# Kernel optimization log

Hardware: AMD Instinct MI355X
Metric: run time of the kernel (lower is better)

## Reference

```python
import jax, jax.numpy as jnp
import numpy as np
import math

B, T, C = 2, 2048, 1024
H, DK, DV = 16, 64, 64


def setup_inputs() -> dict:
    key = jax.random.key(0)
    ks = jax.random.split(key, 5)
    # randw(*d) = randn(*d) / sqrt(d[-1])
    x = jax.random.normal(ks[0], (B, T, C), dtype=jnp.float32)
    w_q = jax.random.normal(ks[1], (H, DK, C), dtype=jnp.float32) / math.sqrt(C)
    w_k = jax.random.normal(ks[2], (H, DK, C), dtype=jnp.float32) / math.sqrt(C)
    w_v = jax.random.normal(ks[3], (H, DV, C), dtype=jnp.float32) / math.sqrt(C)
    w_o = jax.random.normal(ks[4], (H * DV, C), dtype=jnp.float32) / math.sqrt(C)
    return {"x": x, "w_q": w_q, "w_k": w_k, "w_v": w_v, "w_o": w_o}


def reference(x, w_q, w_k, w_v, w_o):
    # Full prefill: bs_q.first = 0, bs_q.nb = T, causal=True, dropout=0 (eval).
    dk = w_q.shape[1]
    q = jnp.einsum('ntc,hdc->nhtd', x, w_q)  # [B,H,T,DK]
    k = jnp.einsum('ntc,hdc->nhtd', x, w_k)  # [B,H,T,DK]
    v = jnp.einsum('ntc,hdc->nhtd', x, w_v)  # [B,H,T,DV]
    a = jnp.einsum('nhtd,nhsd->nhts', q, k) / jnp.sqrt(jnp.asarray(dk, x.dtype))
    # amm_generator: mask where query_idx < key_idx (strict upper triangle)
    t = a.shape[-1]
    mask = jnp.arange(t)[:, None] < jnp.arange(t)[None, :]  # [T,T] bool
    a = jnp.where(mask[None, None], jnp.asarray(-jnp.inf, a.dtype), a)
    a = jax.nn.softmax(a, axis=-1)
    y = jnp.einsum('nhts,nhsd->nthd', a, v)  # [B,T,H,DV]
    y = y.reshape(y.shape[0], y.shape[1], -1)  # [B,T,H*DV]
    return y @ w_o  # [B,T,C]
```

## Files before the change

kernel.cpp:

```cpp
#include <hip/hip_runtime.h>
#include <hip/hip_bf16.h>

#define B_ 2
#define T_ 2048
#define C_ 1024
#define H_ 16
#define D_ 64

typedef __attribute__((ext_vector_type(8))) short bf16x8;
typedef __attribute__((ext_vector_type(4))) float f32x4;
typedef __attribute__((ext_vector_type(8))) unsigned short u16x8;
typedef __attribute__((ext_vector_type(2))) unsigned int u32x2;
typedef __attribute__((ext_vector_type(4))) unsigned int u32x4;

__device__ __forceinline__ unsigned short bf1(float a) {
    __bf16 x = (__bf16)a;
    return __builtin_bit_cast(unsigned short, x);
}
__device__ __forceinline__ unsigned int pk2(float a, float b) {
    return (unsigned int)bf1(a) | ((unsigned int)bf1(b) << 16);
}
__device__ __forceinline__ float bf2f(unsigned short u) {
    union { unsigned int u; float f; } v; v.u = (unsigned int)u << 16;
    return v.f;
}

__device__ __forceinline__ void gll16(const void* g, void* l) {
    __builtin_amdgcn_global_load_lds(
        (const __attribute__((address_space(1))) unsigned int*)g,
        (__attribute__((address_space(3))) unsigned int*)l, 16, 0, 0);
}

__global__ __launch_bounds__(256) void prep_all(
    const float* __restrict__ x, const float* __restrict__ wq,
    const float* __restrict__ wk, const float* __restrict__ wv,
    unsigned short* __restrict__ xb, unsigned short* __restrict__ wb)
{
    const int bid = blockIdx.x, tid = threadIdx.x;
    if (bid < 1024) {
        const size_t i = ((size_t)bid * 256 + tid) * 16;
        float4 f0 = *reinterpret_cast<const float4*>(x + i);
        float4 f1 = *reinterpret_cast<const float4*>(x + i + 4);
        float4 f2 = *reinterpret_cast<const float4*>(x + i + 8);
        float4 f3 = *reinterpret_cast<const float4*>(x + i + 12);
        u32x4 a = {pk2(f0.x, f0.y), pk2(f0.z, f0.w), pk2(f1.x, f1.y), pk2(f1.z, f1.w)};
        u32x4 b = {pk2(f2.x, f2.y), pk2(f2.z, f2.w), pk2(f3.x, f3.y), pk2(f3.z, f3.w)};
        *reinterpret_cast<u32x4*>(xb + i) = a;
        *reinterpret_cast<u32x4*>(xb + i + 8) = b;
    } else {
        const int rb = (bid - 1024) * 4;
        const float* src = (rb < 1024) ? wq + (size_t)rb * 1024
                         : (rb < 2048) ? wk + (size_t)(rb - 1024) * 1024
                                       : wv + (size_t)(rb - 2048) * 1024;
        const float sc = (rb < 1024) ? 0.125f * 1.4426950408889634f : 1.0f;
        const float4* s4 = (const float4*)src;
        u32x2* d = (u32x2*)(wb + (size_t)rb * 1024);
#pragma unroll
        for (int k = 0; k < 4; k++) {
            float4 v = s4[k * 256 + tid];
            u32x2 w;
            w[0] = pk2(v.x * sc, v.y * sc);
            w[1] = pk2(v.z * sc, v.w * sc);
            d[k * 256 + tid] = w;
        }
    }
}

__global__ __launch_bounds__(256) void qkv_gemm(
    const unsigned short* __restrict__ xb, const unsigned short* __restrict__ wb,
    unsigned short* __restrict__ qkv)
{
    __shared__ __align__(16) unsigned short As[128 * 32];
    __shared__ __align__(16) unsigned short Bs[128 * 32];
    const int tid = threadIdx.x;
    const int lane = tid & 63, wave = tid >> 6;
    const int g = lane >> 4, c16 = lane & 15;
    const int xcd = blockIdx.x & 7, idx = blockIdx.x >> 3;
    const int bm = (xcd << 2) + idx / 24, bn = idx % 24;
    const int jbase = bn << 7;
    const int which = jbase >> 10;

    const int srow = lane >> 2, sch = (lane & 3) << 3;
    const unsigned short* asrc = xb + ((size_t)(bm << 7) + wave * 32 + srow) * C_ + sch;
    const unsigned short* bsrc = wb + ((size_t)(bn << 7) + wave * 32 + srow) * C_ + sch;

    f32x4 acc[4][4];
#pragma unroll
    for (int i = 0; i < 4; i++)
#pragma unroll
        for (int j = 0; j < 4; j++) acc[i][j] = (f32x4){0.f, 0.f, 0.f, 0.f};

    const int wm = (wave >> 1) << 6, wn = (wave & 1) << 6;

    for (int t = 0; t < 32; ++t) {
        const int k0 = t << 5;
        __syncthreads();
        gll16(asrc + k0,           &As[(wave * 32) << 5]);
        gll16(asrc + k0 + 16 * C_, &As[(wave * 32 + 16) << 5]);
        gll16(bsrc + k0,           &Bs[(wave * 32) << 5]);
        gll16(bsrc + k0 + 16 * C_, &Bs[(wave * 32 + 16) << 5]);
        __syncthreads();

        bf16x8 af[4], bfv[4];
#pragma unroll
        for (int m = 0; m < 4; m++)
            af[m] = *reinterpret_cast<const bf16x8*>(&As[((wm + m * 16 + c16) << 5) + g * 8]);
#pragma unroll
        for (int n = 0; n < 4; n++)
            bfv[n] = *reinterpret_cast<const bf16x8*>(&Bs[((wn + n * 16 + c16) << 5) + g * 8]);
#pragma unroll
        for (int m = 0; m < 4; m++)
#pragma unroll
            for (int n = 0; n < 4; n++)
                acc[m][n] = __builtin_amdgcn_mfma_f32_16x16x32_bf16(af[m], bfv[n], acc[m][n], 0, 0, 0);
    }

    if (which < 2) {
#pragma unroll
        for (int m = 0; m < 4; m++) {
            const int grow = (bm << 7) + wm + m * 16 + (g << 2);
#pragma unroll
            for (int n = 0; n < 4; n++) {
                const int jj = (jbase + wn + n * 16 + c16) & 1023;
                const int h = jj >> 6, d = jj & 63;
#pragma unroll
                for (int r = 0; r < 4; r++) {
                    const int row = grow + r;
                    const int b = row >> 11, t = row & 2047;
                    const size_t off = ((size_t)((which * B_ + b) * H_ + h) * T_ + t) * 64 + d;
                    qkv[off] = bf1(acc[m][n][r]);
                }
            }
        }
    } else {
#pragma unroll
        for (int m = 0; m < 4; m++) {
            const int grow = (bm << 7) + wm + m * 16 + (g << 2);
            const int b = grow >> 11, t = grow & 2047;
#pragma unroll
            for (int n = 0; n < 4; n++) {
                const int jj = (jbase + wn + n * 16 + c16) & 1023;
                const int h = jj >> 6, d = jj & 63;
                u32x2 w;
                w[0] = pk2(acc[m][n][0], acc[m][n][1]);
                w[1] = pk2(acc[m][n][2], acc[m][n][3]);
                const size_t off = ((size_t)((2 * B_ + b) * H_ + h) * 64 + d) * T_ + t;
                *reinterpret_cast<u32x2*>(&qkv[off]) = w;
            }
        }
    }
}

__global__ __launch_bounds__(256) void attn(
    const unsigned short* __restrict__ qkv,
    unsigned short* __restrict__ opA, unsigned short* __restrict__ opB,
    float* __restrict__ lbuf)
{
    __shared__ __align__(16) unsigned short Ks[64 * 64];
    __shared__ __align__(16) unsigned short Vt[64 * 64];
    __shared__ __align__(16) unsigned short Ps[4][16 * 64];
    const int tid = threadIdx.x, lane = tid & 63, wave = tid >> 6;
    const int g = lane >> 4, c16 = lane & 15;
    const int qt = 31 - (blockIdx.x >> 6);
    const int rem = blockIdx.x & 63;
    const int half = rem >> 5, bh = rem & 31;
    const int b = bh >> 4, h = bh & 15;
    const size_t headoff = (size_t)(b * H_ + h) * T_ * 64;
    const size_t QSZ = (size_t)B_ * H_ * T_ * 64;
    const unsigned short* qp = qkv + headoff;
    const unsigned short* kp = qkv + QSZ + headoff;
    const unsigned short* vTp = qkv + 2 * QSZ + headoff;

    const int nt = qt + 1;
    const int h1 = (nt + 1) >> 1;
    const int itlo = half ? h1 : 0, ithi = half ? nt : h1;

    const int qb = (qt << 6) + wave * 16;
    bf16x8 qf0, qf1;
    {
        const size_t r0 = (size_t)(qb + c16) * 64;
        qf0 = *reinterpret_cast<const bf16x8*>(qp + r0 + g * 8);
        qf1 = *reinterpret_cast<const bf16x8*>(qp + r0 + 32 + g * 8);
    }

    const bf16x8 ones = {0x3F80, 0x3F80, 0x3F80, 0x3F80, 0x3F80, 0x3F80, 0x3F80, 0x3F80};
    f32x4 lacc = (f32x4){0.f, 0.f, 0.f, 0.f};
    f32x4 acc[4];
#pragma unroll
    for (int i = 0; i < 4; i++) acc[i] = (f32x4){0.f, 0.f, 0.f, 0.f};

    const int sw = c16 & 7;
    const int rdo0 = (c16 << 6) + ((g ^ sw) << 3);
    const int rdo1 = (c16 << 6) + (((g + 4) ^ sw) << 3);
    const unsigned short* kr0 = Ks + rdo0;
    const unsigned short* kr1 = Ks + rdo1;
    const unsigned short* vr0 = Vt + rdo0;
    const unsigned short* vr1 = Vt + rdo1;
    const unsigned short* par0 = Ps[wave] + rdo0;
    const unsigned short* par1 = Ps[wave] + rdo1;
    unsigned short* pw[4];
#pragma unroll
    for (int f = 0; f < 4; f++)
        pw[f] = Ps[wave] + (c16 << 6)
              + (((((f << 1) + (g >> 1))) ^ sw) << 3) + ((g & 1) << 2);

    const int srow8 = lane >> 3;
    const int swc = ((lane & 7) ^ srow8) << 3;
    const unsigned short* ksrc = kp + (size_t)(wave * 16 + srow8) * 64 + swc;
    const unsigned short* vsrc = vTp + (size_t)(wave * 16 + srow8) * T_ + swc;

    for (int it = itlo; it < ithi; ++it) {
        const int s0 = it << 6;
        __syncthreads();
#pragma unroll
        for (int i = 0; i < 2; i++) {
            gll16(ksrc + (size_t)(s0 + i * 8) * 64, &Ks[(wave * 16 + i * 8) << 6]);
            gll16(vsrc + s0 + (size_t)i * 8 * T_, &Vt[(wave * 16 + i * 8) << 6]);
        }
        __syncthreads();

        f32x4 sfT[4];
#pragma unroll
        for (int f = 0; f < 4; f++) sfT[f] = (f32x4){-16.f, -16.f, -16.f, -16.f};
        __builtin_amdgcn_s_setprio(1);
#pragma unroll
        for (int f = 0; f < 4; f++) {
            bf16x8 k0 = *reinterpret_cast<const bf16x8*>(kr0 + f * 1024);
            bf16x8 k1 = *reinterpret_cast<const bf16x8*>(kr1 + f * 1024);
            sfT[f] = __builtin_amdgcn_mfma_f32_16x16x32_bf16(k0, qf0, sfT[f], 0, 0, 0);
            sfT[f] = __builtin_amdgcn_mfma_f32_16x16x32_bf16(k1, qf1, sfT[f], 0, 0, 0);
        }
        __builtin_amdgcn_s_setprio(0);

        if (it == qt) {
            const int qg = qb + c16;
#pragma unroll
            for (int f = 0; f < 4; f++)
#pragma unroll
                for (int r = 0; r < 4; r++) {
                    const int kv = s0 + f * 16 + g * 4 + r;
                    if (kv > qg) sfT[f][r] = -1e30f;
                }
        }

#pragma unroll
        for (int f = 0; f < 4; f++)
#pragma unroll
            for (int r = 0; r < 4; r++)
                sfT[f][r] = __builtin_amdgcn_exp2f(sfT[f][r]);

#pragma unroll
        for (int f = 0; f < 4; f++) {
            u32x2 w;
            w[0] = pk2(sfT[f][0], sfT[f][1]);
            w[1] = pk2(sfT[f][2], sfT[f][3]);
            *reinterpret_cast<u32x2*>(pw[f]) = w;
        }

        __builtin_amdgcn_s_setprio(1);
#pragma unroll
        for (int ks = 0; ks < 2; ks++) {
            bf16x8 pa = *reinterpret_cast<const bf16x8*>(ks ? par1 : par0);
            const unsigned short* vp = ks ? vr1 : vr0;
            lacc = __builtin_amdgcn_mfma_f32_16x16x32_bf16(ones, pa, lacc, 0, 0, 0);
#pragma unroll
            for (int fd = 0; fd < 4; fd++) {
                bf16x8 vf = *reinterpret_cast<const bf16x8*>(vp + fd * 1024);
                acc[fd] = __builtin_amdgcn_mfma_f32_16x16x32_bf16(vf, pa, acc[fd], 0, 0, 0);
            }
        }
        __builtin_amdgcn_s_setprio(0);
    }

    unsigned short* op = half ? opB : opA;
#pragma unroll
    for (int fd = 0; fd < 4; fd++) {
        u32x2 w;
        w[0] = pk2(acc[fd][0], acc[fd][1]);
        w[1] = pk2(acc[fd][2], acc[fd][3]);
        const size_t cy = ((size_t)b * T_ + qb + c16) * 1024 + h * 64 + fd * 16 + g * 4;
        *reinterpret_cast<u32x2*>(&op[cy]) = w;
    }
    if (lane < 16)
        lbuf[(size_t)half * (B_ * H_ * T_) + ((size_t)(b * H_ + h)) * T_ + qb + c16] = lacc[0];
}

__global__ __launch_bounds__(256) void combine_wo(
    const unsigned short* __restrict__ opA, const unsigned short* __restrict__ opB,
    const float* __restrict__ lbuf, unsigned short* __restrict__ y,
    const float* __restrict__ wo, unsigned short* __restrict__ wt)
{
    __shared__ unsigned short tile[64][72];
    const int bid = blockIdx.x, tid = threadIdx.x;
    if (bid < 2048) {
        const size_t i = ((size_t)bid * 256 + tid) * 8;
        const int hh = (int)((i >> 6) & 15);
        const int t = (int)((i >> 10) & 2047);
        const int bb = (int)(i >> 21);
        const size_t li = ((size_t)(bb * H_ + hh)) * T_ + t;
        const float inv = 1.0f / (lbuf[li] + lbuf[(size_t)B_ * H_ * T_ + li]);
        u16x8 a = *reinterpret_cast<const u16x8*>(opA + i);
        u16x8 c = *reinterpret_cast<const u16x8*>(opB + i);
        unsigned short o[8];
#pragma unroll
        for (int j = 0; j < 8; j++) o[j] = bf1((bf2f(a[j]) + bf2f(c[j])) * inv);
        *reinterpret_cast<u16x8*>(y + i) = *reinterpret_cast<u16x8*>(o);
    } else {
        const int wb2 = bid - 2048;
        const int tk = (wb2 & 15) << 6, tn = (wb2 >> 4) << 6;
        const int r = tid >> 2, cb = (tid & 3) << 4;
#pragma unroll
        for (int j = 0; j < 4; j++) {
            float4 v = *reinterpret_cast<const float4*>(
                wo + (size_t)(tk + r) * 1024 + tn + cb + j * 4);
            u32x2 w;
            w[0] = pk2(v.x, v.y);
            w[1] = pk2(v.z, v.w);
            *reinterpret_cast<u32x2*>(&tile[r][cb + j * 4]) = w;
        }
        __syncthreads();
        unsigned short buf[16];
#pragma unroll
        for (int j = 0; j < 16; j++) buf[j] = tile[cb + j][r];
        unsigned short* dst = wt + (size_t)(tn + r) * 1024 + tk + cb;
        *reinterpret_cast<u16x8*>(dst) = *reinterpret_cast<u16x8*>(buf);
        *reinterpret_cast<u16x8*>(dst + 8) = *reinterpret_cast<u16x8*>(buf + 8);
    }
}

__global__ __launch_bounds__(256) void out_proj(
    const unsigned short* __restrict__ y, const unsigned short* __restrict__ wt,
    float* __restrict__ out)
{
    __shared__ __align__(16) unsigned short As[128 * 32];
    __shared__ __align__(16) unsigned short Bs[64 * 32];
    const int tid = threadIdx.x;
    const int lane = tid & 63, wave = tid >> 6;
    const int g = lane >> 4, c16 = lane & 15;
    const int xcd = blockIdx.x & 7, idx = blockIdx.x >> 3;
    const int bm = (xcd << 2) + (idx >> 4), bn = idx & 15;
    const int wm = (wave >> 1) << 6, wn = (wave & 1) << 5;

    const int srow = lane >> 2, sch = (lane & 3) << 3;
    const unsigned short* ysrc = y + ((size_t)(bm << 7) + wave * 32 + srow) * 1024 + sch;
    const unsigned short* wsrc = wt + ((size_t)(bn << 6) + wave * 16 + srow) * 1024 + sch;

    f32x4 acc[4][2];
#pragma unroll
    for (int i = 0; i < 4; i++)
#pragma unroll
        for (int j = 0; j < 2; j++) acc[i][j] = (f32x4){0.f, 0.f, 0.f, 0.f};

    for (int t = 0; t < 32; ++t) {
        const int k0 = t << 5;
        __syncthreads();
        gll16(ysrc + k0,             &As[(wave * 32) << 5]);
        gll16(ysrc + k0 + 16 * 1024, &As[(wave * 32 + 16) << 5]);
        gll16(wsrc + k0,             &Bs[(wave * 16) << 5]);
        __syncthreads();

        bf16x8 af[4], bfr[2];
#pragma unroll
        for (int m = 0; m < 4; m++)
            af[m] = *reinterpret_cast<const bf16x8*>(&As[((wm + m * 16 + c16) << 5) + g * 8]);
#pragma unroll
        for (int n = 0; n < 2; n++)
            bfr[n] = *reinterpret_cast<const bf16x8*>(&Bs[((wn + n * 16 + c16) << 5) + g * 8]);
#pragma unroll
        for (int m = 0; m < 4; m++)
#pragma unroll
            for (int n = 0; n < 2; n++)
                acc[m][n] = __builtin_amdgcn_mfma_f32_16x16x32_bf16(af[m], bfr[n], acc[m][n], 0, 0, 0);
    }

#pragma unroll
    for (int m = 0; m < 4; m++) {
        const int grow = (bm << 7) + wm + m * 16 + (g << 2);
#pragma unroll
        for (int n = 0; n < 2; n++) {
            const int gcol = (bn << 6) + wn + n * 16 + c16;
#pragma unroll
            for (int r = 0; r < 4; r++)
                out[(size_t)(grow + r) * 1024 + gcol] = acc[m][n][r];
        }
    }
}

extern "C" void kernel_launch(void* const* d_in, const int* in_sizes, int n_in,
                              void* d_out, int out_size, void* d_ws, size_t ws_size,
                              hipStream_t stream) {
    const float* x  = (const float*)d_in[0];
    const float* wq = (const float*)d_in[1];
    const float* wk = (const float*)d_in[2];
    const float* wv = (const float*)d_in[3];
    const float* wo = (const float*)d_in[4];
    float* out = (float*)d_out;

    unsigned short* wb   = (unsigned short*)d_ws;
    unsigned short* opB  = (unsigned short*)d_ws;
    unsigned short* y    = opB;
    unsigned short* qkv  = (unsigned short*)d_ws + (size_t)4 * 1024 * 1024;
    unsigned short* wt   = qkv;
    unsigned short* xb   = (unsigned short*)d_out;
    unsigned short* opA  = (unsigned short*)d_out;
    float* lbuf = (float*)((char*)d_out + (size_t)8 * 1024 * 1024);

    prep_all<<<dim3(1792), 256, 0, stream>>>(x, wq, wk, wv, xb, wb);
    qkv_gemm<<<dim3(768), 256, 0, stream>>>(xb, wb, qkv);
    attn<<<dim3(2048), 256, 0, stream>>>(qkv, opA, opB, lbuf);
    combine_wo<<<dim3(2048 + 256), 256, 0, stream>>>(opA, opB, lbuf, y, wo, wt);
    out_proj<<<dim3(512), 256, 0, stream>>>(y, wt, out);
}
```

Measured before the change: 107.5 us.

## Use 32x32 MFMA with 128-row query tiles in causal attention

The attention kernel moves from 16x16x32 to 32x32x16 MFMA. Each block now covers 128 query rows with 32 per wave, so each K/V tile loaded into LDS serves twice as many queries, and the grid halves to 1024 blocks. The row-sum is accumulated per lane in registers and reduced with one shuffle, replacing the extra MFMA against a vector of ones. The KV range is split into two causal halves per block, and waves whose rows lie entirely before a tile skip its compute, which adds some wave imbalance and lower occupancy from the larger accumulators.

```diff
diff --git a/kernel.cpp b/kernel.cpp
--- a/kernel.cpp
+++ b/kernel.cpp
@@ -9,6 +9,7 @@
 
 typedef __attribute__((ext_vector_type(8))) short bf16x8;
 typedef __attribute__((ext_vector_type(4))) float f32x4;
+typedef __attribute__((ext_vector_type(16))) float f32x16;
 typedef __attribute__((ext_vector_type(8))) unsigned short u16x8;
 typedef __attribute__((ext_vector_type(2))) unsigned int u32x2;
 typedef __attribute__((ext_vector_type(4))) unsigned int u32x4;
@@ -158,12 +159,12 @@
 {
     __shared__ __align__(16) unsigned short Ks[64 * 64];
     __shared__ __align__(16) unsigned short Vt[64 * 64];
-    __shared__ __align__(16) unsigned short Ps[4][16 * 64];
-    const int tid = threadIdx.x, lane = tid & 63, wave = tid >> 6;
-    const int g = lane >> 4, c16 = lane & 15;
-    const int qt = 31 - (blockIdx.x >> 6);
+    __shared__ __align__(16) unsigned short Ps[4][32 * 64];
+    const int tid = threadIdx.x, lane = tid & 63, w = tid >> 6;
+    const int l31 = lane & 31, lh = lane >> 5;
+    const int qt = 15 - (blockIdx.x >> 6);
     const int rem = blockIdx.x & 63;
-    const int half = rem >> 5, bh = rem & 31;
+    const int split = rem >> 5, bh = rem & 31;
     const int b = bh >> 4, h = bh & 15;
     const size_t headoff = (size_t)(b * H_ + h) * T_ * 64;
     const size_t QSZ = (size_t)B_ * H_ * T_ * 64;
@@ -171,118 +172,123 @@
     const unsigned short* kp = qkv + QSZ + headoff;
     const unsigned short* vTp = qkv + 2 * QSZ + headoff;
 
-    const int nt = qt + 1;
-    const int h1 = (nt + 1) >> 1;
-    const int itlo = half ? h1 : 0, ithi = half ? nt : h1;
-
-    const int qb = (qt << 6) + wave * 16;
-    bf16x8 qf0, qf1;
-    {
-        const size_t r0 = (size_t)(qb + c16) * 64;
-        qf0 = *reinterpret_cast<const bf16x8*>(qp + r0 + g * 8);
-        qf1 = *reinterpret_cast<const bf16x8*>(qp + r0 + 32 + g * 8);
-    }
-
-    const bf16x8 ones = {0x3F80, 0x3F80, 0x3F80, 0x3F80, 0x3F80, 0x3F80, 0x3F80, 0x3F80};
-    f32x4 lacc = (f32x4){0.f, 0.f, 0.f, 0.f};
-    f32x4 acc[4];
-#pragma unroll
-    for (int i = 0; i < 4; i++) acc[i] = (f32x4){0.f, 0.f, 0.f, 0.f};
-
-    const int sw = c16 & 7;
-    const int rdo0 = (c16 << 6) + ((g ^ sw) << 3);
-    const int rdo1 = (c16 << 6) + (((g + 4) ^ sw) << 3);
-    const unsigned short* kr0 = Ks + rdo0;
-    const unsigned short* kr1 = Ks + rdo1;
-    const unsigned short* vr0 = Vt + rdo0;
-    const unsigned short* vr1 = Vt + rdo1;
-    const unsigned short* par0 = Ps[wave] + rdo0;
-    const unsigned short* par1 = Ps[wave] + rdo1;
-    unsigned short* pw[4];
+    const int itlo = split ? (qt + 1) : 0;
+    const int ithi = split ? (2 * qt + 2) : (qt + 1);
+
+    const int qb = (qt << 7) + w * 32;
+    const int qg = qb + l31;
+
+    bf16x8 qf[4];
 #pragma unroll
     for (int f = 0; f < 4; f++)
-        pw[f] = Ps[wave] + (c16 << 6)
-              + (((((f << 1) + (g >> 1))) ^ sw) << 3) + ((g & 1) << 2);
+        qf[f] = *reinterpret_cast<const bf16x8*>(qp + (size_t)qg * 64 + f * 16 + lh * 8);
+
+    f32x16 oacc[2];
+#pragma unroll
+    for (int i = 0; i < 16; i++) { oacc[0][i] = 0.f; oacc[1][i] = 0.f; }
+    float l_lane = 0.f;
+
+    const int cx = l31 & 7;
+    const unsigned short* kbase = Ks + (l31 << 6);
+    const unsigned short* vbase = Vt + (l31 << 6);
+    const unsigned short* prb = Ps[w] + (l31 << 6);
+    unsigned short* pwb = Ps[w] + (l31 << 6);
 
     const int srow8 = lane >> 3;
     const int swc = ((lane & 7) ^ srow8) << 3;
-    const unsigned short* ksrc = kp + (size_t)(wave * 16 + srow8) * 64 + swc;
-    const unsigned short* vsrc = vTp + (size_t)(wave * 16 + srow8) * T_ + swc;
+    const unsigned short* ksrc = kp + (size_t)(w * 16 + srow8) * 64 + swc;
+    const unsigned short* vsrc = vTp + (size_t)(w * 16 + srow8) * T_ + swc;
 
     for (int it = itlo; it < ithi; ++it) {
         const int s0 = it << 6;
         __syncthreads();
 #pragma unroll
         for (int i = 0; i < 2; i++) {
-            gll16(ksrc + (size_t)(s0 + i * 8) * 64, &Ks[(wave * 16 + i * 8) << 6]);
-            gll16(vsrc + s0 + (size_t)i * 8 * T_, &Vt[(wave * 16 + i * 8) << 6]);
-        }
-        __syncthreads();
-
-        f32x4 sfT[4];
-#pragma unroll
-        for (int f = 0; f < 4; f++) sfT[f] = (f32x4){-16.f, -16.f, -16.f, -16.f};
+            gll16(ksrc + (size_t)(s0 + i * 8) * 64, &Ks[(w * 16 + i * 8) << 6]);
+            gll16(vsrc + s0 + (size_t)i * 8 * T_, &Vt[(w * 16 + i * 8) << 6]);
+        }
+        __syncthreads();
+
+        if (s0 > qb + 31) continue;
+
+        f32x16 sq[2];
+#pragma unroll
+        for (int i = 0; i < 16; i++) { sq[0][i] = -16.f; sq[1][i] = -16.f; }
         __builtin_amdgcn_s_setprio(1);
 #pragma unroll
-        for (int f = 0; f < 4; f++) {
-            bf16x8 k0 = *reinterpret_cast<const bf16x8*>(kr0 + f * 1024);
-            bf16x8 k1 = *reinterpret_cast<const bf16x8*>(kr1 + f * 1024);
-            sfT[f] = __builtin_amdgcn_mfma_f32_16x16x32_bf16(k0, qf0, sfT[f], 0, 0, 0);
-            sfT[f] = __builtin_amdgcn_mfma_f32_16x16x32_bf16(k1, qf1, sfT[f], 0, 0, 0);
+        for (int kf = 0; kf < 2; kf++) {
+#pragma unroll
+            for (int f = 0; f < 4; f++) {
+                bf16x8 ka = *reinterpret_cast<const bf16x8*>(
+                    kbase + (kf << 11) + ((((f << 1) + lh) ^ cx) << 3));
+                sq[kf] = __builtin_amdgcn_mfma_f32_32x32x16_bf16(ka, qf[f], sq[kf], 0, 0, 0);
+            }
         }
         __builtin_amdgcn_s_setprio(0);
 
-        if (it == qt) {
-            const int qg = qb + c16;
-#pragma unroll
-            for (int f = 0; f < 4; f++)
-#pragma unroll
-                for (int r = 0; r < 4; r++) {
-                    const int kv = s0 + f * 16 + g * 4 + r;
-                    if (kv > qg) sfT[f][r] = -1e30f;
+        if (s0 + 63 > qb) {
+#pragma unroll
+            for (int kf = 0; kf < 2; kf++)
+#pragma unroll
+                for (int r = 0; r < 16; r++) {
+                    const int kv = s0 + (kf << 5) + (r & 3) + ((r >> 2) << 3) + (lh << 2);
+                    if (kv > qg) sq[kf][r] = -1e30f;
                 }
         }
 
 #pragma unroll
-        for (int f = 0; f < 4; f++)
-#pragma unroll
-            for (int r = 0; r < 4; r++)
-                sfT[f][r] = __builtin_amdgcn_exp2f(sfT[f][r]);
-
-#pragma unroll
-        for (int f = 0; f < 4; f++) {
-            u32x2 w;
-            w[0] = pk2(sfT[f][0], sfT[f][1]);
-            w[1] = pk2(sfT[f][2], sfT[f][3]);
-            *reinterpret_cast<u32x2*>(pw[f]) = w;
-        }
-
+        for (int kf = 0; kf < 2; kf++)
+#pragma unroll
+            for (int r = 0; r < 16; r++) {
+                const float pv = __builtin_amdgcn_exp2f(sq[kf][r]);
+                sq[kf][r] = pv;
+                l_lane += pv;
+            }
+
+#pragma unroll
+        for (int kf = 0; kf < 2; kf++)
+#pragma unroll
+            for (int rr = 0; rr < 4; rr++) {
+                u32x2 wv;
+                wv[0] = pk2(sq[kf][4 * rr], sq[kf][4 * rr + 1]);
+                wv[1] = pk2(sq[kf][4 * rr + 2], sq[kf][4 * rr + 3]);
+                *reinterpret_cast<u32x2*>(
+                    pwb + ((((kf << 2) + rr) ^ cx) << 3) + (lh << 2)) = wv;
+            }
+
+        bf16x8 pB[4];
+#pragma unroll
+        for (int kf2 = 0; kf2 < 4; kf2++)
+            pB[kf2] = *reinterpret_cast<const bf16x8*>(
+                prb + ((((kf2 << 1) + lh) ^ cx) << 3));
         __builtin_amdgcn_s_setprio(1);
 #pragma unroll
-        for (int ks = 0; ks < 2; ks++) {
-            bf16x8 pa = *reinterpret_cast<const bf16x8*>(ks ? par1 : par0);
-            const unsigned short* vp = ks ? vr1 : vr0;
-            lacc = __builtin_amdgcn_mfma_f32_16x16x32_bf16(ones, pa, lacc, 0, 0, 0);
-#pragma unroll
-            for (int fd = 0; fd < 4; fd++) {
-                bf16x8 vf = *reinterpret_cast<const bf16x8*>(vp + fd * 1024);
-                acc[fd] = __builtin_amdgcn_mfma_f32_16x16x32_bf16(vf, pa, acc[fd], 0, 0, 0);
+        for (int df = 0; df < 2; df++) {
+#pragma unroll
+            for (int kf2 = 0; kf2 < 4; kf2++) {
+                bf16x8 va = *reinterpret_cast<const bf16x8*>(
+                    vbase + (df << 11) + ((((kf2 << 1) + lh) ^ cx) << 3));
+                oacc[df] = __builtin_amdgcn_mfma_f32_32x32x16_bf16(va, pB[kf2], oacc[df], 0, 0, 0);
             }
         }
         __builtin_amdgcn_s_setprio(0);
     }
 
-    unsigned short* op = half ? opB : opA;
-#pragma unroll
-    for (int fd = 0; fd < 4; fd++) {
-        u32x2 w;
-        w[0] = pk2(acc[fd][0], acc[fd][1]);
-        w[1] = pk2(acc[fd][2], acc[fd][3]);
-        const size_t cy = ((size_t)b * T_ + qb + c16) * 1024 + h * 64 + fd * 16 + g * 4;
-        *reinterpret_cast<u32x2*>(&op[cy]) = w;
-    }
-    if (lane < 16)
-        lbuf[(size_t)half * (B_ * H_ * T_) + ((size_t)(b * H_ + h)) * T_ + qb + c16] = lacc[0];
+    unsigned short* op = split ? opB : opA;
+    const size_t orow = ((size_t)b * T_ + qg) * 1024 + h * 64;
+#pragma unroll
+    for (int df = 0; df < 2; df++)
+#pragma unroll
+        for (int rr = 0; rr < 4; rr++) {
+            const int d = (df << 5) + (rr << 3) + (lh << 2);
+            u32x2 wv;
+            wv[0] = pk2(oacc[df][4 * rr], oacc[df][4 * rr + 1]);
+            wv[1] = pk2(oacc[df][4 * rr + 2], oacc[df][4 * rr + 3]);
+            *reinterpret_cast<u32x2*>(&op[orow + d]) = wv;
+        }
+    l_lane += __shfl_xor(l_lane, 32, 64);
+    if (lane < 32)
+        lbuf[(size_t)split * (B_ * H_ * T_) + ((size_t)(b * H_ + h)) * T_ + qg] = l_lane;
 }
 
 __global__ __launch_bounds__(256) void combine_wo(
@@ -407,7 +413,7 @@
 
     prep_all<<<dim3(1792), 256, 0, stream>>>(x, wq, wk, wv, xb, wb);
     qkv_gemm<<<dim3(768), 256, 0, stream>>>(xb, wb, qkv);
-    attn<<<dim3(2048), 256, 0, stream>>>(qkv, opA, opB, lbuf);
+    attn<<<dim3(1024), 256, 0, stream>>>(qkv, opA, opB, lbuf);
     combine_wo<<<dim3(2048 + 256), 256, 0, stream>>>(opA, opB, lbuf, y, wo, wt);
     out_proj<<<dim3(512), 256, 0, stream>>>(y, wt, out);
 }
```

After: 107.5 us. No clear change (-0.0%).
